# Optimization experiments

Measured on AMD Instinct MI355X. Metric: run time of the kernel, lower is better.

Reference implementation:

```python
import jax, jax.numpy as jnp
import numpy as np

N_NODES = 50000
N_EDGES = 800000
D_FEAT = 128
N_LAYERS = 3
HALF = 64  # units // 2 per kernel in tf_geometric MeanGraphSage
HIDDEN = 256
NUM_LABELS = 40


def setup_inputs() -> dict:
    key = jax.random.key(0)
    ks = jax.random.split(key, 6)
    x = jax.random.normal(ks[0], (N_NODES, D_FEAT), dtype=jnp.float32)
    edge_index = jax.random.randint(ks[1], (2, N_EDGES), 0, N_NODES, dtype=jnp.int32)
    self_kernels = jax.random.normal(ks[2], (N_LAYERS, D_FEAT, HALF), dtype=jnp.float32) * 0.05
    neighbor_kernels = jax.random.normal(ks[3], (N_LAYERS, D_FEAT, HALF), dtype=jnp.float32) * 0.05
    biases = jnp.zeros((N_LAYERS, 2 * HALF), dtype=jnp.float32)
    mlp_w1 = jax.random.normal(ks[4], (2 * HALF, HIDDEN), dtype=jnp.float32) * 0.05
    mlp_b1 = jnp.zeros((HIDDEN,), dtype=jnp.float32)
    mlp_w2 = jax.random.normal(ks[5], (HIDDEN, NUM_LABELS), dtype=jnp.float32) * 0.05
    mlp_b2 = jnp.zeros((NUM_LABELS,), dtype=jnp.float32)
    return {"x": x, "edge_index": edge_index, "self_kernels": self_kernels,
            "neighbor_kernels": neighbor_kernels, "biases": biases,
            "mlp_w1": mlp_w1, "mlp_b1": mlp_b1, "mlp_w2": mlp_w2, "mlp_b2": mlp_b2}


def reference(x, edge_index, self_kernels, neighbor_kernels, biases,
              mlp_w1, mlp_b1, mlp_w2, mlp_b2):
    n = x.shape[0]
    row, col = edge_index[0], edge_index[1]  # row: target node, col: source node
    # in-degree counts (graph is fixed across layers)
    ones = jnp.ones((edge_index.shape[1],), dtype=x.dtype)
    deg = jax.ops.segment_sum(ones, row, num_segments=n)  # [N]
    inv_deg = (1.0 / jnp.maximum(deg, 1.0))[:, None]      # [N,1]

    h = x
    for i in range(N_LAYERS):
        # mean-neighbor aggregation: gather source feats, segment-sum to targets
        nbr_sum = jax.ops.segment_sum(h[col], row, num_segments=n)  # [N,D]
        nbr_mean = nbr_sum * inv_deg
        from_self = h @ self_kernels[i]        # [N,HALF]
        from_nbr = nbr_mean @ neighbor_kernels[i]  # [N,HALF]
        h = jax.nn.relu(jnp.concatenate([from_self, from_nbr], axis=1) + biases[i])

    # MLP head (Flatten on [N,128] is a no-op)
    h = jax.nn.relu(h @ mlp_w1 + mlp_b1)
    return h @ mlp_w2 + mlp_b2
```

## Files before the change

kernel.cpp:

```cpp
#include <hip/hip_runtime.h>
#include <hip/hip_bf16.h>
#include <hip/hip_fp16.h>
#include <cstdint>
#include <cstddef>

#define N_NODES 50000
#define N_PAD   50176
#define N_EDGES 800000
#define D_FEAT  128
#define HALF    64
#define HIDDEN  256
#define LABELS  40

#define NBUCK 196
#define BCAP  5632
#define EDGES_PER_BLK 4096

#define HID_STRIDE 264

typedef __attribute__((ext_vector_type(8))) short bf16x8;
typedef __attribute__((ext_vector_type(4))) float f32x4;

#define PK_SELF(L) ((size_t)(L) * 8192)
#define PK_NBR(L)  (24576 + (size_t)(L) * 8192)
#define PK_W1      49152
#define PK_W2      81920
#define PK_TOTAL   94208

__device__ inline uint16_t f2bf_bits(float f) {
    __hip_bfloat16 b = __float2bfloat16(f);
    uint16_t u; __builtin_memcpy(&u, &b, 2); return u;
}

__device__ inline float2 h2f(uint32_t u) {
    __half2 h; __builtin_memcpy(&h, &u, 4);
    return __half22float2(h);
}

__global__ __launch_bounds__(1024) void bucket_scatter_kernel(
        const int* __restrict__ row, const int* __restrict__ col,
        int* __restrict__ bucket_cursor, uint32_t* __restrict__ staged) {
    __shared__ int hist[NBUCK];
    __shared__ int hbase[NBUCK];
    int tid  = threadIdx.x;
    int e0   = blockIdx.x * EDGES_PER_BLK;
    int eend = e0 + EDGES_PER_BLK; if (eend > N_EDGES) eend = N_EDGES;

    for (int i = tid; i < NBUCK; i += 1024) hist[i] = 0;
    __syncthreads();

    int rr[4], cc[4]; int ne = 0;
    for (int e = e0 + tid; e < eend; e += 1024) {
        rr[ne] = row[e]; cc[ne] = col[e]; ne++;
    }
    for (int i = 0; i < ne; i++) atomicAdd(&hist[rr[i] >> 8], 1);
    __syncthreads();

    for (int i = tid; i < NBUCK; i += 1024) {
        hbase[i] = atomicAdd(&bucket_cursor[i], hist[i]);
        hist[i]  = 0;
    }
    __syncthreads();

    for (int i = 0; i < ne; i++) {
        int b   = rr[i] >> 8;
        int off = atomicAdd(&hist[b], 1);
        int pos = hbase[b] + off;
        if (pos < BCAP)
            staged[(size_t)b * BCAP + pos] =
                ((uint32_t)(rr[i] & 255) << 16) | (uint32_t)cc[i];
    }
}

__global__ __launch_bounds__(1024) void bucket_fill_kernel(
        const uint32_t* __restrict__ staged, const int* __restrict__ bucket_cursor,
        int* __restrict__ deg, int* __restrict__ rowstart,
        float* __restrict__ inv_deg, uint16_t* __restrict__ csr_col) {
    __shared__ int cnt[256];
    __shared__ int excl[256];
    __shared__ int wt[4];
    __shared__ int seg[BCAP];
    __shared__ int base_s;
    int b   = blockIdx.x;
    int tid = threadIdx.x;

    if (tid < 64) {
        int partial = 0;
        for (int i = tid; i < b; i += 64) partial += bucket_cursor[i];
#pragma unroll
        for (int off = 32; off > 0; off >>= 1)
            partial += __shfl_down(partial, off, 64);
        if (tid == 0) base_s = partial;
    }
    if (tid < 256) cnt[tid] = 0;
    __syncthreads();

    int total = bucket_cursor[b]; if (total > BCAP) total = BCAP;
    int gbase = base_s;
    const uint32_t* st = staged + (size_t)b * BCAP;

    for (int i = tid; i < total; i += 1024) atomicAdd(&cnt[st[i] >> 16], 1);
    __syncthreads();

    int lane = tid & 63, wid = tid >> 6;
    int v = 0, s = 0;
    if (tid < 256) {
        v = cnt[tid]; s = v;
#pragma unroll
        for (int off = 1; off < 64; off <<= 1) {
            int t = __shfl_up(s, off, 64);
            if (lane >= off) s += t;
        }
        if (lane == 63) wt[wid] = s;
    }
    __syncthreads();
    if (tid == 0) { int a = 0; for (int i = 0; i < 4; i++) { int t = wt[i]; wt[i] = a; a += t; } }
    __syncthreads();
    if (tid < 256) {
        int ex = s - v + wt[wid];
        excl[tid] = ex;
        int node = (b << 8) + tid;
        if (node < N_NODES) {
            deg[node]      = v;
            rowstart[node] = gbase + ex;
            inv_deg[node]  = 1.0f / fmaxf((float)v, 1.0f);
        }
    }
    __syncthreads();
    for (int i = tid; i < total; i += 1024) {
        uint32_t u = st[i];
        int p = atomicAdd(&excl[u >> 16], 1);
        seg[p] = (int)(u & 0xffffu);
    }
    __syncthreads();
    for (int i = tid; i < total; i += 1024)
        csr_col[gbase + i] = (uint16_t)seg[i];
}

__global__ __launch_bounds__(256) void pack_all_kernel(
        const float* __restrict__ selfk, const float* __restrict__ nbrk,
        const float* __restrict__ w1, const float* __restrict__ w2,
        __hip_bfloat16* __restrict__ wpack) {
    int m = blockIdx.y;
    const float* W; int K, Ncols, Npad; size_t dstoff;
    if (m < 3)      { W = selfk + (size_t)m*D_FEAT*HALF;      K=128; Ncols=64;  Npad=64;  dstoff = PK_SELF(m); }
    else if (m < 6) { W = nbrk  + (size_t)(m-3)*D_FEAT*HALF;  K=128; Ncols=64;  Npad=64;  dstoff = PK_NBR(m-3); }
    else if (m == 6){ W = w1;                                 K=128; Ncols=256; Npad=256; dstoff = PK_W1; }
    else            { W = w2;                                 K=256; Ncols=40;  Npad=48;  dstoff = PK_W2; }
    int ksteps = K / 32;
    int total  = ksteps * (Npad / 16) * 64;
    int t = blockIdx.x * blockDim.x + threadIdx.x;
    if (t >= total) return;
    int lane = t & 63;
    int rest = t >> 6;
    int ks   = rest % ksteps;
    int ns   = rest / ksteps;
    int colb = ns * 16 + (lane & 15);
    int kb   = ks * 32 + (lane >> 4) * 8;
    __hip_bfloat16* dst = wpack + dstoff + (size_t)t * 8;
#pragma unroll
    for (int j = 0; j < 8; j++) {
        float v = (colb < Ncols) ? W[(size_t)(kb + j) * Ncols + colb] : 0.f;
        dst[j] = __float2bfloat16(v);
    }
}

template<bool AF32>
__global__ __launch_bounds__(256, 2) void layer_gemm_kernel(
        const void* __restrict__ Ain,
        const __hip_bfloat16* __restrict__ wpack_self,
        const __hip_bfloat16* __restrict__ wpack_nbr,
        const float* __restrict__ bias,
        __hip_bfloat16* __restrict__ hout,
        uint16_t* __restrict__ zn) {
    int wave = threadIdx.x >> 6, lane = threadIdx.x & 63;
    int row0 = blockIdx.x * 128 + wave * 32;
    int lrow = lane & 15, lgrp = lane >> 4;

    const __hip_bfloat16 *hr0 = nullptr, *hr1 = nullptr;
    const float *xr0 = nullptr, *xr1 = nullptr;
    if constexpr (AF32) {
        const float* x = (const float*)Ain;
        int r0 = min(row0 + lrow, N_NODES - 1);
        int r1 = min(row0 + lrow + 16, N_NODES - 1);
        xr0 = x + (size_t)r0 * D_FEAT + lgrp * 8;
        xr1 = x + (size_t)r1 * D_FEAT + lgrp * 8;
    } else {
        const __hip_bfloat16* h = (const __hip_bfloat16*)Ain;
        hr0 = h + (size_t)(row0 + lrow) * D_FEAT + lgrp * 8;
        hr1 = hr0 + (size_t)16 * D_FEAT;
    }

    f32x4 accS[2][4] = {};
    f32x4 accN[2][4] = {};
#pragma unroll
    for (int ks = 0; ks < 4; ks++) {
        bf16x8 a0, a1;
        if constexpr (AF32) {
            float4 u0  = *(const float4*)(xr0 + ks * 32);
            float4 u0b = *(const float4*)(xr0 + ks * 32 + 4);
            float4 u1  = *(const float4*)(xr1 + ks * 32);
            float4 u1b = *(const float4*)(xr1 + ks * 32 + 4);
            float f0[8] = {u0.x, u0.y, u0.z, u0.w, u0b.x, u0b.y, u0b.z, u0b.w};
            float f1[8] = {u1.x, u1.y, u1.z, u1.w, u1b.x, u1b.y, u1b.z, u1b.w};
#pragma unroll
            for (int j = 0; j < 8; j++) { a0[j] = (short)f2bf_bits(f0[j]); a1[j] = (short)f2bf_bits(f1[j]); }
        } else {
            a0 = *(const bf16x8*)(hr0 + ks * 32);
            a1 = *(const bf16x8*)(hr1 + ks * 32);
        }
#pragma unroll
        for (int ns = 0; ns < 4; ns++) {
            bf16x8 bs = *(const bf16x8*)(wpack_self + ((size_t)(ns * 4 + ks) * 64 + lane) * 8);
            accS[0][ns] = __builtin_amdgcn_mfma_f32_16x16x32_bf16(a0, bs, accS[0][ns], 0, 0, 0);
            accS[1][ns] = __builtin_amdgcn_mfma_f32_16x16x32_bf16(a1, bs, accS[1][ns], 0, 0, 0);
            bf16x8 bn = *(const bf16x8*)(wpack_nbr + ((size_t)(ns * 4 + ks) * 64 + lane) * 8);
            accN[0][ns] = __builtin_amdgcn_mfma_f32_16x16x32_bf16(a0, bn, accN[0][ns], 0, 0, 0);
            accN[1][ns] = __builtin_amdgcn_mfma_f32_16x16x32_bf16(a1, bn, accN[1][ns], 0, 0, 0);
        }
    }
#pragma unroll
    for (int t = 0; t < 2; t++) {
#pragma unroll
        for (int ns = 0; ns < 4; ns++) {
            int colS = ns * 16 + lrow;
            float bvS = bias[colS];
#pragma unroll
            for (int i = 0; i < 4; i++) {
                int r = row0 + t * 16 + lgrp * 4 + i;
                hout[(size_t)r * D_FEAT + colS] =
                    __float2bfloat16(fmaxf(accS[t][ns][i] + bvS, 0.f));
                __half hz = __float2half(accN[t][ns][i]);
                uint16_t hb; __builtin_memcpy(&hb, &hz, 2);
                zn[(size_t)r * HALF + colS] = hb;
            }
        }
    }
}

__global__ __launch_bounds__(128) void agg8_kernel(
        const uint16_t* __restrict__ zn, const uint16_t* __restrict__ csr_col,
        const int* __restrict__ rowstart, const int* __restrict__ deg,
        const float* __restrict__ inv_deg, const float* __restrict__ bias64,
        __hip_bfloat16* __restrict__ hout) {
    int gid  = blockIdx.x * 128 + threadIdx.x;
    int wnum = gid >> 6;
    int lane = threadIdx.x & 63;
    int sub  = lane >> 3;
    int sl   = lane & 7;
    int node = wnum * 8 + sub;
    int start = rowstart[node];
    int d     = deg[node];
    const uint32_t* zw = (const uint32_t*)zn;
    float acc[8] = {};

#define ACC8H(U) {                                                      \
    float2 t0 = h2f((U).x); acc[0] += t0.x; acc[1] += t0.y;             \
    float2 t1 = h2f((U).y); acc[2] += t1.x; acc[3] += t1.y;             \
    float2 t2 = h2f((U).z); acc[4] += t2.x; acc[5] += t2.y;             \
    float2 t3 = h2f((U).w); acc[6] += t3.x; acc[7] += t3.y; }

    if (d > 0) {
        int last = start + d - 1;
        int s[8];
#pragma unroll
        for (int k = 0; k < 8; k++) s[k] = csr_col[min(start + k, last)];
        int j = 0;
        for (; j + 8 <= d; j += 8) {
            int p[8];
#pragma unroll
            for (int k = 0; k < 8; k++) p[k] = csr_col[min(start + j + 8 + k, last)];
            uint4 u0 = *(const uint4*)(zw + (size_t)s[0] * 32 + sl * 4);
            uint4 u1 = *(const uint4*)(zw + (size_t)s[1] * 32 + sl * 4);
            uint4 u2 = *(const uint4*)(zw + (size_t)s[2] * 32 + sl * 4);
            uint4 u3 = *(const uint4*)(zw + (size_t)s[3] * 32 + sl * 4);
            uint4 u4 = *(const uint4*)(zw + (size_t)s[4] * 32 + sl * 4);
            uint4 u5 = *(const uint4*)(zw + (size_t)s[5] * 32 + sl * 4);
            uint4 u6 = *(const uint4*)(zw + (size_t)s[6] * 32 + sl * 4);
            uint4 u7 = *(const uint4*)(zw + (size_t)s[7] * 32 + sl * 4);
            ACC8H(u0); ACC8H(u1); ACC8H(u2); ACC8H(u3);
            ACC8H(u4); ACC8H(u5); ACC8H(u6); ACC8H(u7);
#pragma unroll
            for (int k = 0; k < 8; k++) s[k] = p[k];
        }
        int r = d - j;
#pragma unroll
        for (int k = 0; k < 8; k++) {
            if (k < r) {
                uint4 u = *(const uint4*)(zw + (size_t)s[k] * 32 + sl * 4);
                ACC8H(u);
            }
        }
    }
#undef ACC8H

    float inv = inv_deg[node];
    const float* bb = bias64 + sl * 8;
    float4 b0 = *(const float4*)bb;
    float4 b1 = *(const float4*)(bb + 4);
    uint4 p;
    p.x = (uint32_t)f2bf_bits(fmaxf(acc[0] * inv + b0.x, 0.f))
        | ((uint32_t)f2bf_bits(fmaxf(acc[1] * inv + b0.y, 0.f)) << 16);
    p.y = (uint32_t)f2bf_bits(fmaxf(acc[2] * inv + b0.z, 0.f))
        | ((uint32_t)f2bf_bits(fmaxf(acc[3] * inv + b0.w, 0.f)) << 16);
    p.z = (uint32_t)f2bf_bits(fmaxf(acc[4] * inv + b1.x, 0.f))
        | ((uint32_t)f2bf_bits(fmaxf(acc[5] * inv + b1.y, 0.f)) << 16);
    p.w = (uint32_t)f2bf_bits(fmaxf(acc[6] * inv + b1.z, 0.f))
        | ((uint32_t)f2bf_bits(fmaxf(acc[7] * inv + b1.w, 0.f)) << 16);
    *(uint4*)((uint32_t*)hout + (size_t)node * 64 + 32 + sl * 4) = p;
}

__global__ __launch_bounds__(256, 2) void mlp_fused_kernel(
        const __hip_bfloat16* __restrict__ h, const __hip_bfloat16* __restrict__ w1p,
        const float* __restrict__ b1, const __hip_bfloat16* __restrict__ w2p,
        const float* __restrict__ b2, float* __restrict__ out) {
    __shared__ __align__(16) uint16_t hid[128 * HID_STRIDE];
    int wave = threadIdx.x >> 6, lane = threadIdx.x & 63;
    int row0 = blockIdx.x * 128 + wave * 32;
    int lrow = lane & 15, lgrp = lane >> 4;

    {
        const __hip_bfloat16* ar0 = h + (size_t)(row0 + lrow) * D_FEAT + lgrp * 8;
        const __hip_bfloat16* ar1 = ar0 + (size_t)16 * D_FEAT;
        f32x4 acc[2][16] = {};
#pragma unroll 1
        for (int ks = 0; ks < 4; ks++) {
            bf16x8 a0 = *(const bf16x8*)(ar0 + ks * 32);
            bf16x8 a1 = *(const bf16x8*)(ar1 + ks * 32);
#pragma unroll
            for (int ns = 0; ns < 16; ns++) {
                bf16x8 bfr = *(const bf16x8*)(w1p + ((size_t)(ns * 4 + ks) * 64 + lane) * 8);
                acc[0][ns] = __builtin_amdgcn_mfma_f32_16x16x32_bf16(a0, bfr, acc[0][ns], 0, 0, 0);
                acc[1][ns] = __builtin_amdgcn_mfma_f32_16x16x32_bf16(a1, bfr, acc[1][ns], 0, 0, 0);
            }
        }
        int lbase = wave * 32;
#pragma unroll
        for (int t = 0; t < 2; t++) {
#pragma unroll
            for (int ns = 0; ns < 16; ns++) {
                int col = ns * 16 + lrow;
                float bv = b1[col];
#pragma unroll
                for (int i = 0; i < 4; i++) {
                    int lr = lbase + t * 16 + lgrp * 4 + i;
                    hid[lr * HID_STRIDE + col] =
                        f2bf_bits(fmaxf(acc[t][ns][i] + bv, 0.f));
                }
            }
        }
    }
    __syncthreads();

    const uint16_t* br0 = &hid[(wave * 32 + lrow) * HID_STRIDE + lgrp * 8];
    const uint16_t* br1 = br0 + 16 * HID_STRIDE;
    f32x4 acc2[2][3] = {};
#pragma unroll
    for (int ks = 0; ks < 8; ks++) {
        bf16x8 a0 = *(const bf16x8*)(br0 + ks * 32);
        bf16x8 a1 = *(const bf16x8*)(br1 + ks * 32);
#pragma unroll
        for (int ns = 0; ns < 3; ns++) {
            bf16x8 bfr = *(const bf16x8*)(w2p + ((size_t)(ns * 8 + ks) * 64 + lane) * 8);
            acc2[0][ns] = __builtin_amdgcn_mfma_f32_16x16x32_bf16(a0, bfr, acc2[0][ns], 0, 0, 0);
            acc2[1][ns] = __builtin_amdgcn_mfma_f32_16x16x32_bf16(a1, bfr, acc2[1][ns], 0, 0, 0);
        }
    }
#pragma unroll
    for (int t = 0; t < 2; t++) {
#pragma unroll
        for (int ns = 0; ns < 3; ns++) {
            int col = ns * 16 + lrow;
            if (col < LABELS) {
                float bv = b2[col];
#pragma unroll
                for (int i = 0; i < 4; i++) {
                    int r = row0 + t * 16 + lgrp * 4 + i;
                    if (r < N_NODES)
                        out[(size_t)r * LABELS + col] = acc2[t][ns][i] + bv;
                }
            }
        }
    }
}

extern "C" void kernel_launch(void* const* d_in, const int* in_sizes, int n_in,
                              void* d_out, int out_size, void* d_ws, size_t ws_size,
                              hipStream_t stream) {
    const float* x      = (const float*)d_in[0];
    const int*   ei     = (const int*)d_in[1];
    const float* selfk  = (const float*)d_in[2];
    const float* nbrk   = (const float*)d_in[3];
    const float* biases = (const float*)d_in[4];
    const float* w1     = (const float*)d_in[5];
    const float* b1     = (const float*)d_in[6];
    const float* w2     = (const float*)d_in[7];
    const float* b2     = (const float*)d_in[8];
    float* out = (float*)d_out;

    const int* row = ei;
    const int* col = ei + N_EDGES;

    char* ws = (char*)d_ws;
    size_t off = 0;
    auto alloc = [&](size_t bytes) -> char* {
        char* p = ws + off;
        off = (off + bytes + 255) & ~(size_t)255;
        return p;
    };
    int*   deg       = (int*)  alloc((size_t)N_NODES * 4);
    int*   rowstart  = (int*)  alloc((size_t)N_NODES * 4);
    float* inv_deg   = (float*)alloc((size_t)N_NODES * 4);
    int*   bucket_cursor = (int*)alloc(256 * 4);
    uint16_t* csr_col = (uint16_t*)alloc((size_t)N_EDGES * 2);
    uint32_t* staged = (uint32_t*)alloc((size_t)NBUCK * BCAP * 4);
    __hip_bfloat16* wpack  = (__hip_bfloat16*)alloc(PK_TOTAL * 2);
    __hip_bfloat16* hA     = (__hip_bfloat16*)alloc((size_t)N_PAD * D_FEAT * 2);
    __hip_bfloat16* hB     = (__hip_bfloat16*)alloc((size_t)N_PAD * D_FEAT * 2);
    uint16_t*       zn     = (uint16_t*)alloc((size_t)N_PAD * HALF * 2);

    hipMemsetAsync(bucket_cursor, 0, 256 * 4, stream);

    const int scat_blocks = (N_EDGES + EDGES_PER_BLK - 1) / EDGES_PER_BLK;
    bucket_scatter_kernel<<<scat_blocks, 1024, 0, stream>>>(row, col, bucket_cursor, staged);
    bucket_fill_kernel<<<NBUCK, 1024, 0, stream>>>(staged, bucket_cursor,
                                                   deg, rowstart, inv_deg, csr_col);

    dim3 pgrid(16, 8);
    pack_all_kernel<<<pgrid, 256, 0, stream>>>(selfk, nbrk, w1, w2, wpack);

    const int layer_blocks = N_PAD / 128;
    const int agg_blocks   = N_NODES / 16;

    layer_gemm_kernel<true><<<layer_blocks, 256, 0, stream>>>(
        (const void*)x, wpack + PK_SELF(0), wpack + PK_NBR(0), biases, hA, zn);
    agg8_kernel<<<agg_blocks, 128, 0, stream>>>(zn, csr_col, rowstart, deg,
                                                inv_deg, biases + 64, hA);
    layer_gemm_kernel<false><<<layer_blocks, 256, 0, stream>>>(
        (const void*)hA, wpack + PK_SELF(1), wpack + PK_NBR(1), biases + 128, hB, zn);
    agg8_kernel<<<agg_blocks, 128, 0, stream>>>(zn, csr_col, rowstart, deg,
                                                inv_deg, biases + 128 + 64, hB);
    layer_gemm_kernel<false><<<layer_blocks, 256, 0, stream>>>(
        (const void*)hB, wpack + PK_SELF(2), wpack + PK_NBR(2), biases + 256, hA, zn);
    agg8_kernel<<<agg_blocks, 128, 0, stream>>>(zn, csr_col, rowstart, deg,
                                                inv_deg, biases + 256 + 64, hA);

    mlp_fused_kernel<<<layer_blocks, 256, 0, stream>>>(hA, wpack + PK_W1, b1,
                                                       wpack + PK_W2, b2, out);
}
```

Before: 207.2 us.

## Fuse CSR bucket fill with first-layer GEMM into one heterogeneous launch

Merges the bucket_fill kernel (CSR build, degree and inv_deg) and the layer-0 GEMM into a single 392-block launch. The first 196 blocks run the GEMM with 512 threads covering 256 rows each, and the remaining 196 blocks build the CSR buckets. This removes one launch and lets the two independent stages overlap on the GPU. In exchange, every GEMM block now reserves the fill stage's large static shared memory, which can lower occupancy, and the fill loops use a 512 stride instead of 1024.

```diff
diff --git a/kernel.cpp b/kernel.cpp
--- a/kernel.cpp
+++ b/kernel.cpp
@@ -70,71 +70,6 @@
             staged[(size_t)b * BCAP + pos] =
                 ((uint32_t)(rr[i] & 255) << 16) | (uint32_t)cc[i];
     }
-}
-
-__global__ __launch_bounds__(1024) void bucket_fill_kernel(
-        const uint32_t* __restrict__ staged, const int* __restrict__ bucket_cursor,
-        int* __restrict__ deg, int* __restrict__ rowstart,
-        float* __restrict__ inv_deg, uint16_t* __restrict__ csr_col) {
-    __shared__ int cnt[256];
-    __shared__ int excl[256];
-    __shared__ int wt[4];
-    __shared__ int seg[BCAP];
-    __shared__ int base_s;
-    int b   = blockIdx.x;
-    int tid = threadIdx.x;
-
-    if (tid < 64) {
-        int partial = 0;
-        for (int i = tid; i < b; i += 64) partial += bucket_cursor[i];
-#pragma unroll
-        for (int off = 32; off > 0; off >>= 1)
-            partial += __shfl_down(partial, off, 64);
-        if (tid == 0) base_s = partial;
-    }
-    if (tid < 256) cnt[tid] = 0;
-    __syncthreads();
-
-    int total = bucket_cursor[b]; if (total > BCAP) total = BCAP;
-    int gbase = base_s;
-    const uint32_t* st = staged + (size_t)b * BCAP;
-
-    for (int i = tid; i < total; i += 1024) atomicAdd(&cnt[st[i] >> 16], 1);
-    __syncthreads();
-
-    int lane = tid & 63, wid = tid >> 6;
-    int v = 0, s = 0;
-    if (tid < 256) {
-        v = cnt[tid]; s = v;
-#pragma unroll
-        for (int off = 1; off < 64; off <<= 1) {
-            int t = __shfl_up(s, off, 64);
-            if (lane >= off) s += t;
-        }
-        if (lane == 63) wt[wid] = s;
-    }
-    __syncthreads();
-    if (tid == 0) { int a = 0; for (int i = 0; i < 4; i++) { int t = wt[i]; wt[i] = a; a += t; } }
-    __syncthreads();
-    if (tid < 256) {
-        int ex = s - v + wt[wid];
-        excl[tid] = ex;
-        int node = (b << 8) + tid;
-        if (node < N_NODES) {
-            deg[node]      = v;
-            rowstart[node] = gbase + ex;
-            inv_deg[node]  = 1.0f / fmaxf((float)v, 1.0f);
-        }
-    }
-    __syncthreads();
-    for (int i = tid; i < total; i += 1024) {
-        uint32_t u = st[i];
-        int p = atomicAdd(&excl[u >> 16], 1);
-        seg[p] = (int)(u & 0xffffu);
-    }
-    __syncthreads();
-    for (int i = tid; i < total; i += 1024)
-        csr_col[gbase + i] = (uint16_t)seg[i];
 }
 
 __global__ __launch_bounds__(256) void pack_all_kernel(
@@ -166,15 +101,12 @@
 }
 
 template<bool AF32>
-__global__ __launch_bounds__(256, 2) void layer_gemm_kernel(
-        const void* __restrict__ Ain,
+__device__ inline void gemm_wave_body(
+        const void* __restrict__ Ain, int row0, int lane,
         const __hip_bfloat16* __restrict__ wpack_self,
         const __hip_bfloat16* __restrict__ wpack_nbr,
         const float* __restrict__ bias,
-        __hip_bfloat16* __restrict__ hout,
-        uint16_t* __restrict__ zn) {
-    int wave = threadIdx.x >> 6, lane = threadIdx.x & 63;
-    int row0 = blockIdx.x * 128 + wave * 32;
+        __hip_bfloat16* __restrict__ hout, uint16_t* __restrict__ zn) {
     int lrow = lane & 15, lgrp = lane >> 4;
 
     const __hip_bfloat16 *hr0 = nullptr, *hr1 = nullptr;
@@ -236,6 +168,96 @@
             }
         }
     }
+}
+
+__global__ __launch_bounds__(256, 2) void layer_gemm_kernel(
+        const void* __restrict__ Ain,
+        const __hip_bfloat16* __restrict__ wpack_self,
+        const __hip_bfloat16* __restrict__ wpack_nbr,
+        const float* __restrict__ bias,
+        __hip_bfloat16* __restrict__ hout, uint16_t* __restrict__ zn) {
+    int wave = threadIdx.x >> 6, lane = threadIdx.x & 63;
+    int row0 = blockIdx.x * 128 + wave * 32;
+    gemm_wave_body<false>(Ain, row0, lane, wpack_self, wpack_nbr, bias, hout, zn);
+}
+
+__global__ __launch_bounds__(512, 2) void gemm0_fill_kernel(
+        const float* __restrict__ x,
+        const __hip_bfloat16* __restrict__ wpack_self,
+        const __hip_bfloat16* __restrict__ wpack_nbr,
+        const float* __restrict__ bias,
+        __hip_bfloat16* __restrict__ hout, uint16_t* __restrict__ zn,
+        const uint32_t* __restrict__ staged, const int* __restrict__ bucket_cursor,
+        int* __restrict__ deg, int* __restrict__ rowstart,
+        float* __restrict__ inv_deg, uint16_t* __restrict__ csr_col) {
+    __shared__ int cnt[256];
+    __shared__ int excl[256];
+    __shared__ int wt[4];
+    __shared__ int seg[BCAP];
+    __shared__ int base_s;
+
+    if (blockIdx.x < 196) {
+        int wave = threadIdx.x >> 6, lane = threadIdx.x & 63;
+        int row0 = blockIdx.x * 256 + wave * 32;
+        gemm_wave_body<true>((const void*)x, row0, lane,
+                             wpack_self, wpack_nbr, bias, hout, zn);
+        return;
+    }
+
+    int b   = blockIdx.x - 196;
+    int tid = threadIdx.x;
+
+    if (tid < 64) {
+        int partial = 0;
+        for (int i = tid; i < b; i += 64) partial += bucket_cursor[i];
+#pragma unroll
+        for (int off = 32; off > 0; off >>= 1)
+            partial += __shfl_down(partial, off, 64);
+        if (tid == 0) base_s = partial;
+    }
+    if (tid < 256) cnt[tid] = 0;
+    __syncthreads();
+
+    int total = bucket_cursor[b]; if (total > BCAP) total = BCAP;
+    int gbase = base_s;
+    const uint32_t* st = staged + (size_t)b * BCAP;
+
+    for (int i = tid; i < total; i += 512) atomicAdd(&cnt[st[i] >> 16], 1);
+    __syncthreads();
+
+    int lane = tid & 63, wid = tid >> 6;
+    int v = 0, s = 0;
+    if (tid < 256) {
+        v = cnt[tid]; s = v;
+#pragma unroll
+        for (int off = 1; off < 64; off <<= 1) {
+            int t = __shfl_up(s, off, 64);
+            if (lane >= off) s += t;
+        }
+        if (lane == 63) wt[wid] = s;
+    }
+    __syncthreads();
+    if (tid == 0) { int a = 0; for (int i = 0; i < 4; i++) { int t = wt[i]; wt[i] = a; a += t; } }
+    __syncthreads();
+    if (tid < 256) {
+        int ex = s - v + wt[wid];
+        excl[tid] = ex;
+        int node = (b << 8) + tid;
+        if (node < N_NODES) {
+            deg[node]      = v;
+            rowstart[node] = gbase + ex;
+            inv_deg[node]  = 1.0f / fmaxf((float)v, 1.0f);
+        }
+    }
+    __syncthreads();
+    for (int i = tid; i < total; i += 512) {
+        uint32_t u = st[i];
+        int p = atomicAdd(&excl[u >> 16], 1);
+        seg[p] = (int)(u & 0xffffu);
+    }
+    __syncthreads();
+    for (int i = tid; i < total; i += 512)
+        csr_col[gbase + i] = (uint16_t)seg[i];
 }
 
 __global__ __launch_bounds__(128) void agg8_kernel(
@@ -423,8 +445,6 @@
 
     const int scat_blocks = (N_EDGES + EDGES_PER_BLK - 1) / EDGES_PER_BLK;
     bucket_scatter_kernel<<<scat_blocks, 1024, 0, stream>>>(row, col, bucket_cursor, staged);
-    bucket_fill_kernel<<<NBUCK, 1024, 0, stream>>>(staged, bucket_cursor,
-                                                   deg, rowstart, inv_deg, csr_col);
 
     dim3 pgrid(16, 8);
     pack_all_kernel<<<pgrid, 256, 0, stream>>>(selfk, nbrk, w1, w2, wpack);
@@ -432,15 +452,16 @@
     const int layer_blocks = N_PAD / 128;
     const int agg_blocks   = N_NODES / 16;
 
-    layer_gemm_kernel<true><<<layer_blocks, 256, 0, stream>>>(
-        (const void*)x, wpack + PK_SELF(0), wpack + PK_NBR(0), biases, hA, zn);
+    gemm0_fill_kernel<<<392, 512, 0, stream>>>(
+        x, wpack + PK_SELF(0), wpack + PK_NBR(0), biases, hA, zn,
+        staged, bucket_cursor, deg, rowstart, inv_deg, csr_col);
     agg8_kernel<<<agg_blocks, 128, 0, stream>>>(zn, csr_col, rowstart, deg,
                                                 inv_deg, biases + 64, hA);
-    layer_gemm_kernel<false><<<layer_blocks, 256, 0, stream>>>(
+    layer_gemm_kernel<<<layer_blocks, 256, 0, stream>>>(
         (const void*)hA, wpack + PK_SELF(1), wpack + PK_NBR(1), biases + 128, hB, zn);
     agg8_kernel<<<agg_blocks, 128, 0, stream>>>(zn, csr_col, rowstart, deg,
                                                 inv_deg, biases + 128 + 64, hB);
-    layer_gemm_kernel<false><<<layer_blocks, 256, 0, stream>>>(
+    layer_gemm_kernel<<<layer_blocks, 256, 0, stream>>>(
         (const void*)hB, wpack + PK_SELF(2), wpack + PK_NBR(2), biases + 256, hA, zn);
     agg8_kernel<<<agg_blocks, 128, 0, stream>>>(zn, csr_col, rowstart, deg,
                                                 inv_deg, biases + 256 + 64, hA);
```

Measured after the change: 198.7 us (median of 2 runs). 1.04x faster.
